# Kernel optimization log

Measured on AMD Instinct MI355X. Metric: run time of the kernel, lower is better.

Reference implementation:

```python
import jax, jax.numpy as jnp
import numpy as np

EPS = 1e-5

def _ln(t, g, b):
    m = t.mean(-1, keepdims=True)
    v = ((t - m) ** 2).mean(-1, keepdims=True)
    return (t - m) * jax.lax.rsqrt(v + EPS) * g + b

def _sr(t, w, b, H, W, sr):
    # t: [B, H*W, C] -> spatial-reduction conv -> [B, (H//sr)*(W//sr), C]
    B, L, C = t.shape
    xi = t.transpose(0, 2, 1).reshape(B, C, H, W)
    y = jax.lax.conv_general_dilated(xi, w, (sr, sr), 'VALID',
                                     dimension_numbers=('NCHW', 'OIHW', 'NCHW'))
    return y.reshape(B, C, -1).transpose(0, 2, 1) + b

def setup_inputs() -> dict:
    key = jax.random.key(0)
    ks = jax.random.split(key, 9)
    C, head, sr, H, W = 128, 2, 2, 64, 64
    B, N = 4, 2 * H * W
    s = 0.02
    return {
        'x': jax.random.normal(ks[0], (B, N, C), jnp.float32),
        'qW': jax.random.normal(ks[1], (C, C), jnp.float32) * s,
        'qb': jnp.zeros((C,), jnp.float32),
        'kvW': jax.random.normal(ks[2], (C, 2 * C), jnp.float32) * s,
        'kvb': jnp.zeros((2 * C,), jnp.float32),
        'projW': jax.random.normal(ks[3], (C, C), jnp.float32) * s,
        'projb': jnp.zeros((C,), jnp.float32),
        'srW': jax.random.normal(ks[4], (C, C, sr, sr), jnp.float32) * s,
        'srb': jnp.zeros((C,), jnp.float32),
        'lnW': jnp.ones((C,), jnp.float32),
        'lnB': jnp.zeros((C,), jnp.float32),
        'H': H, 'W': W, 'fuse': 1,
    }

def reference(x, qW, qb, kvW, kvb, projW, projb, srW, srb, lnW, lnB, H, W, fuse):
    head, sr = 2, 2
    B, N, C = x.shape
    Dh = C // head
    scale = Dh ** -0.5
    q = (x @ qW + qb).reshape(B, N, head, Dh).transpose(0, 2, 1, 3)  # [B,h,N,Dh]
    mask = None
    if fuse and sr > 1:
        half = N // 2
        x_rgb = _ln(_sr(x[:, :half, :], srW, srb, H, W, sr), lnW, lnB)
        x_dte = _ln(_sr(x[:, half:, :], srW, srb, H, W, sr), lnW, lnB)
        xkv = jnp.concatenate([x_rgb, x_dte], axis=1)
        M = N // (sr * sr)
        row = jnp.arange(N)[:, None] < half            # query in rgb half
        col = jnp.arange(M)[None, :] < (M // 2)        # key in rgb half
        mask = row == col                              # True on same-modality blocks -> masked
    elif sr > 1:
        xkv = _ln(_sr(x, srW, srb, H, W, sr), lnW, lnB)
    else:
        xkv = x
    M = xkv.shape[1]
    kv = (xkv @ kvW + kvb).reshape(B, M, 2, head, Dh).transpose(2, 0, 3, 1, 4)
    k, v = kv[0], kv[1]                                # [B,h,M,Dh]
    attn = jnp.einsum('bhnd,bhmd->bhnm', q, k) * scale
    if mask is not None:
        attn = jnp.where(mask[None, None], -jnp.inf, attn)
    attn = jax.nn.softmax(attn, axis=-1)
    out = jnp.einsum('bhnm,bhmd->bhnd', attn, v).transpose(0, 2, 1, 3).reshape(B, N, C)
    return out @ projW + projb
```

## Files before the change

kernel.cpp:

```cpp
#include <hip/hip_runtime.h>
#include <hip/hip_bf16.h>

#define LN_EPS 1e-5f

typedef __attribute__((ext_vector_type(8))) short bf16x8_t;
typedef __attribute__((ext_vector_type(4))) short bf16x4_t;
typedef __attribute__((ext_vector_type(4))) float f32x4_t;
typedef __attribute__((ext_vector_type(4))) unsigned short u16x4_t;

#define MFMA32(a, b, c) __builtin_amdgcn_mfma_f32_16x16x32_bf16(a, b, c, 0, 0, 0)
#define MFMA16(a, b, c) __builtin_amdgcn_mfma_f32_16x16x16bf16_1k(a, b, c, 0, 0, 0)

__device__ inline unsigned short f2bf(float f) {
    union { float f; unsigned int u; } v; v.f = f;
    unsigned int r = v.u + 0x7fffu + ((v.u >> 16) & 1u);
    return (unsigned short)(r >> 16);
}

__device__ inline u16x4_t pk4(float a, float b, float c, float d) {
    union { u16x4_t v; __hip_bfloat162 h[2]; } u;
    u.h[0] = __float22bfloat162_rn(float2{a, b});
    u.h[1] = __float22bfloat162_rn(float2{c, d});
    return u.v;
}
__device__ inline bf16x4_t pk4b(float a, float b, float c, float d) {
    union { bf16x4_t v; __hip_bfloat162 h[2]; } u;
    u.h[0] = __float22bfloat162_rn(float2{a, b});
    u.h[1] = __float22bfloat162_rn(float2{c, d});
    return u.v;
}
__device__ inline bf16x8_t pk8(float4 a, float4 b) {
    union { bf16x8_t v; __hip_bfloat162 h[4]; } u;
    u.h[0] = __float22bfloat162_rn(float2{a.x, a.y});
    u.h[1] = __float22bfloat162_rn(float2{a.z, a.w});
    u.h[2] = __float22bfloat162_rn(float2{b.x, b.y});
    u.h[3] = __float22bfloat162_rn(float2{b.z, b.w});
    return u.v;
}

__device__ inline size_t fragidx(int row, int k, int KC) {
    return ((size_t)((row >> 4) * KC + (k >> 5))) * 512 +
           (((k >> 3) & 3) * 16 + (row & 15)) * 8 + (k & 7);
}

__global__ void k_prep_w(const float* __restrict__ qW, const float* __restrict__ kvW,
                         const float* __restrict__ projW, const float* __restrict__ srW,
                         unsigned short* __restrict__ qWs, unsigned short* __restrict__ kvWs,
                         unsigned short* __restrict__ projWs, unsigned short* __restrict__ srWs) {
    int i = blockIdx.x * 256 + threadIdx.x;
    if (i < 16384) {
        int n = i & 127, k = i >> 7;
        qWs[fragidx(n, k, 4)] = f2bf(qW[k * 128 + n]);
    } else if (i < 49152) {
        int j = i - 16384; int n = j & 255, k = j >> 8;
        kvWs[fragidx(n, k, 4)] = f2bf(kvW[k * 256 + n]);
    } else if (i < 65536) {
        int j = i - 49152; int n = j & 127, k = j >> 7;
        projWs[fragidx(n, k, 4)] = f2bf(projW[k * 128 + n]);
    } else {
        int j = i - 65536; int n = j >> 9, rem = j & 511, q = rem >> 7, c = rem & 127;
        srWs[fragidx(n, q * 128 + c, 16)] = f2bf(srW[n * 512 + c * 4 + q]);
    }
}

__global__ __launch_bounds__(256)
void k_convkv(const float* __restrict__ x, const unsigned short* __restrict__ srWs,
              const float* __restrict__ srb, const float* __restrict__ lnW,
              const float* __restrict__ lnB, const unsigned short* __restrict__ kvWs,
              const float* __restrict__ kvb, unsigned short* __restrict__ ksw,
              unsigned short* __restrict__ vls) {
    const int t = threadIdx.x, w = t >> 6, lane = t & 63;
    const int col = lane & 15, quad = lane >> 4;
    const int RT = blockIdx.x;

    __shared__ unsigned short xs[4 * 512];
    __shared__ float lnred[4][16][2];

    const int pos = RT * 16 + col;
    const int pb = pos >> 11, phf = (pos >> 10) & 1;
    const int poy = (pos >> 5) & 31, pox = pos & 31;
    int rowbase[4];
    #pragma unroll
    for (int q = 0; q < 4; q++) {
        int ky = q >> 1, kx = q & 1;
        int n = phf * 4096 + (2 * poy + ky) * 64 + 2 * pox + kx;
        rowbase[q] = (pb * 8192 + n) * 128;
    }

    f32x4_t acc[2] = {};
    {
        const unsigned short* wp = srWs + lane * 8;
        #pragma unroll
        for (int kc = 0; kc < 16; kc++) {
            const float* xr = x + rowbase[kc >> 2] + (kc & 3) * 32 + quad * 8;
            float4 xa = *(const float4*)(xr);
            float4 xb2 = *(const float4*)(xr + 4);
            bf16x8_t xb = pk8(xa, xb2);
            #pragma unroll
            for (int jj = 0; jj < 2; jj++) {
                bf16x8_t wf = *(const bf16x8_t*)(wp + (size_t)((w * 2 + jj) * 16 + kc) * 512);
                acc[jj] = MFMA32(wf, xb, acc[jj]);
            }
        }
    }
    float s = 0.f, ss = 0.f;
    #pragma unroll
    for (int jj = 0; jj < 2; jj++) {
        float4 bs = *(const float4*)(srb + (w * 2 + jj) * 16 + quad * 4);
        acc[jj][0] += bs.x; acc[jj][1] += bs.y; acc[jj][2] += bs.z; acc[jj][3] += bs.w;
        #pragma unroll
        for (int r = 0; r < 4; r++) { float v = acc[jj][r]; s += v; ss += v * v; }
    }
    s += __shfl_xor(s, 16, 64);  s += __shfl_xor(s, 32, 64);
    ss += __shfl_xor(ss, 16, 64); ss += __shfl_xor(ss, 32, 64);
    if (lane < 16) { lnred[w][lane][0] = s; lnred[w][lane][1] = ss; }
    __syncthreads();
    float stot = 0.f, sstot = 0.f;
    #pragma unroll
    for (int ww = 0; ww < 4; ww++) { stot += lnred[ww][col][0]; sstot += lnred[ww][col][1]; }
    float mean = stot * (1.0f / 128.0f);
    float var = sstot * (1.0f / 128.0f) - mean * mean;
    float rs = rsqrtf(var + LN_EPS);
    #pragma unroll
    for (int jj = 0; jj < 2; jj++) {
        int f0 = (w * 2 + jj) * 16 + quad * 4;
        float4 g = *(const float4*)(lnW + f0);
        float4 be = *(const float4*)(lnB + f0);
        u16x4_t o = pk4((acc[jj][0] - mean) * rs * g.x + be.x,
                        (acc[jj][1] - mean) * rs * g.y + be.y,
                        (acc[jj][2] - mean) * rs * g.z + be.z,
                        (acc[jj][3] - mean) * rs * g.w + be.w);
        *(u16x4_t*)(xs + ((size_t)(f0 >> 5)) * 512 +
                    (((f0 >> 3) & 3) * 16 + col) * 8 + (f0 & 7)) = o;
    }
    __syncthreads();
    bf16x8_t xf[4];
    #pragma unroll
    for (int kc = 0; kc < 4; kc++)
        xf[kc] = *(const bf16x8_t*)(xs + (size_t)kc * 512 + lane * 8);
    const int p0 = RT * 16;
    const int bb = p0 >> 11;
    #pragma unroll
    for (int jj = 0; jj < 2; jj++) {
        const int nt = w * 2 + jj;
        f32x4_t aK = {};
        #pragma unroll
        for (int kc = 0; kc < 4; kc++) {
            bf16x8_t wf = *(const bf16x8_t*)(kvWs + (size_t)(nt * 4 + kc) * 512 + lane * 8);
            aK = MFMA32(wf, xf[kc], aK);
        }
        float4 bs = *(const float4*)(kvb + nt * 16 + quad * 4);
        int m = (p0 + col) & 2047;
        int bh = bb * 2 + (nt >> 2);
        int d0 = (nt & 3) * 16 + quad * 4;
        u16x4_t o = pk4(aK[0] + bs.x, aK[1] + bs.y, aK[2] + bs.z, aK[3] + bs.w);
        *(u16x4_t*)(ksw + ((size_t)(bh * 128 + (m >> 4)) * 2 + (d0 >> 5)) * 512 +
                    (((d0 >> 3) & 3) * 16 + (m & 15)) * 8 + (d0 & 7)) = o;
    }
    #pragma unroll
    for (int jj = 0; jj < 2; jj++) {
        const int nt = w * 2 + jj;
        f32x4_t aV = {};
        #pragma unroll
        for (int kc = 0; kc < 4; kc++) {
            bf16x8_t wf = *(const bf16x8_t*)(kvWs + (size_t)((8 + nt) * 4 + kc) * 512 + lane * 8);
            aV = MFMA32(xf[kc], wf, aV);
        }
        int fv = nt * 16 + col;
        int h = fv >> 6, dd = fv & 63;
        float bv = kvb[128 + fv];
        int m0 = (p0 + quad * 4) & 2047;
        int bh = bb * 2 + h;
        int kt = m0 >> 6, nb = (m0 >> 4) & 3;
        u16x4_t o = pk4(aV[0] + bv, aV[1] + bv, aV[2] + bv, aV[3] + bv);
        *(u16x4_t*)(vls + (((size_t)(bh * 32 + kt) * 4 + (dd >> 4)) * 2 + (nb >> 1)) * 512 +
                    (quad * 16 + (dd & 15)) * 8 + (nb & 1) * 4) = o;
    }
}

__global__ __launch_bounds__(256)
void k_attn_f3(const float* __restrict__ x, const unsigned short* __restrict__ qWs,
               const float* __restrict__ qb, const unsigned short* __restrict__ ksw,
               const unsigned short* __restrict__ vls, const unsigned short* __restrict__ projWs,
               const float* __restrict__ projb, float* __restrict__ out) {
    const int blkx = blockIdx.x, mod = blockIdx.y, b = blockIdx.z;
    const int t = threadIdx.x, w = t >> 6, lane = t & 63;
    const int col = lane & 15, quad = lane >> 4;
    const int h = w & 1, ks = w >> 1;
    const int bh = b * 2 + h;
    const int qbase = mod * 4096 + blkx * 32;

    __shared__ float Ocomb[2 * 32 * 64];
    __shared__ float lcomb[64];
    __shared__ unsigned short rows[32 * 136];
    __shared__ unsigned short qfr[2 * 4 * 512];

    {
        const int qt = ks;
        const float* xrow = x + ((size_t)b * 8192 + qbase + qt * 16 + col) * 128;
        const float sc = 0.125f * 1.44269504089f;
        f32x4_t acc[4] = {};
        #pragma unroll
        for (int kc = 0; kc < 4; kc++) {
            float4 xa = *(const float4*)(xrow + kc * 32 + quad * 8);
            float4 xb2 = *(const float4*)(xrow + kc * 32 + quad * 8 + 4);
            bf16x8_t xf = pk8(xa, xb2);
            #pragma unroll
            for (int j = 0; j < 4; j++) {
                bf16x8_t wf = *(const bf16x8_t*)(qWs + (size_t)((h * 4 + j) * 4 + kc) * 512 + lane * 8);
                acc[j] = MFMA32(wf, xf, acc[j]);
            }
        }
        #pragma unroll
        for (int j = 0; j < 4; j++) {
            float4 bs = *(const float4*)(qb + h * 64 + j * 16 + quad * 4);
            u16x4_t o = pk4((acc[j][0] + bs.x) * sc, (acc[j][1] + bs.y) * sc,
                            (acc[j][2] + bs.z) * sc, (acc[j][3] + bs.w) * sc);
            *(u16x4_t*)(qfr + (size_t)h * 2048 + ((size_t)(qt * 2 + (j >> 1))) * 512 +
                        (((j & 1) * 2 + (quad >> 1)) * 16 + col) * 8 + (quad & 1) * 4) = o;
        }
    }
    __syncthreads();
    bf16x8_t qf[2][2];
    #pragma unroll
    for (int qt = 0; qt < 2; qt++)
        #pragma unroll
        for (int kc = 0; kc < 2; kc++)
            qf[qt][kc] = *(const bf16x8_t*)(qfr + (size_t)h * 2048 +
                                            (size_t)(qt * 2 + kc) * 512 + lane * 8);

    const unsigned short* kp0 =
        ksw + ((size_t)(bh * 128 + (1 - mod) * 64) * 2) * 512 + lane * 8;
    const unsigned short* vp0 =
        vls + ((size_t)(bh * 32 + (1 - mod) * 16) * 8) * 512 + lane * 8;
    const bf16x4_t ones4 = { 0x3F80, 0x3F80, 0x3F80, 0x3F80 };

    f32x4_t O[2][4] = {};
    f32x4_t accl[2] = {};

    for (int kt = ks * 8; kt < ks * 8 + 8; kt++) {
        bf16x8_t kf[8];
        #pragma unroll
        for (int i = 0; i < 8; i++)
            kf[i] = *(const bf16x8_t*)(kp0 + (size_t)(kt * 8 + i) * 512);
        union { bf16x8_t v8; bf16x4_t v4[2]; } vf[8];
        #pragma unroll
        for (int i = 0; i < 8; i++)
            vf[i].v8 = *(const bf16x8_t*)(vp0 + (size_t)(kt * 8 + i) * 512);
        f32x4_t ST[2][4];
        #pragma unroll
        for (int qt = 0; qt < 2; qt++)
            #pragma unroll
            for (int nb = 0; nb < 4; nb++) {
                f32x4_t sA = {};
                sA = MFMA32(kf[nb * 2 + 0], qf[qt][0], sA);
                sA = MFMA32(kf[nb * 2 + 1], qf[qt][1], sA);
                ST[qt][nb] = sA;
            }
        bf16x4_t pa[2][4];
        #pragma unroll
        for (int qt = 0; qt < 2; qt++)
            #pragma unroll
            for (int nb = 0; nb < 4; nb++)
                pa[qt][nb] = pk4b(exp2f(ST[qt][nb][0]), exp2f(ST[qt][nb][1]),
                                  exp2f(ST[qt][nb][2]), exp2f(ST[qt][nb][3]));
        #pragma unroll
        for (int qt = 0; qt < 2; qt++) {
            #pragma unroll
            for (int nb = 0; nb < 4; nb++) {
                accl[qt] = MFMA16(pa[qt][nb], ones4, accl[qt]);
                #pragma unroll
                for (int dt = 0; dt < 4; dt++)
                    O[qt][dt] = MFMA16(pa[qt][nb], vf[dt * 2 + (nb >> 1)].v4[nb & 1], O[qt][dt]);
            }
        }
    }

    if (ks == 1) {
        #pragma unroll
        for (int qt = 0; qt < 2; qt++)
            #pragma unroll
            for (int r = 0; r < 4; r++) {
                int qrow = qt * 16 + quad * 4 + r;
                #pragma unroll
                for (int dt = 0; dt < 4; dt++)
                    Ocomb[(h * 32 + qrow) * 64 + dt * 16 + col] = O[qt][dt][r];
                if (col == 0) lcomb[h * 32 + qrow] = accl[qt][r];
            }
    }
    __syncthreads();
    if (ks == 0) {
        #pragma unroll
        for (int qt = 0; qt < 2; qt++)
            #pragma unroll
            for (int r = 0; r < 4; r++) {
                int qrow = qt * 16 + quad * 4 + r;
                float lt = accl[qt][r] + lcomb[h * 32 + qrow];
                float rl = 1.0f / lt;
                #pragma unroll
                for (int dt = 0; dt < 4; dt++) {
                    float ov = O[qt][dt][r] + Ocomb[(h * 32 + qrow) * 64 + dt * 16 + col];
                    rows[qrow * 136 + h * 64 + dt * 16 + col] = f2bf(ov * rl);
                }
            }
    }
    __syncthreads();
    if (ks == 0) {
        const int qt2 = h;
        bf16x8_t ob[4];
        #pragma unroll
        for (int kc = 0; kc < 4; kc++)
            ob[kc] = *(const bf16x8_t*)(rows + (size_t)(qt2 * 16 + col) * 136 + kc * 32 + quad * 8);
        f32x4_t acc[8];
        #pragma unroll
        for (int j = 0; j < 8; j++) acc[j] = f32x4_t{};
        #pragma unroll
        for (int kc = 0; kc < 4; kc++)
            #pragma unroll
            for (int j = 0; j < 8; j++) {
                bf16x8_t wf = *(const bf16x8_t*)(projWs + (size_t)(j * 4 + kc) * 512 + lane * 8);
                acc[j] = MFMA32(wf, ob[kc], acc[j]);
            }
        const int n = b * 8192 + qbase + qt2 * 16 + col;
        #pragma unroll
        for (int j = 0; j < 8; j++) {
            int f0 = j * 16 + quad * 4;
            float4 bs = *(const float4*)(projb + f0);
            float4 o = { acc[j][0] + bs.x, acc[j][1] + bs.y,
                         acc[j][2] + bs.z, acc[j][3] + bs.w };
            *(float4*)(out + (size_t)n * 128 + f0) = o;
        }
    }
}

extern "C" void kernel_launch(void* const* d_in, const int* in_sizes, int n_in,
                              void* d_out, int out_size, void* d_ws, size_t ws_size,
                              hipStream_t stream) {
    const float* x     = (const float*)d_in[0];
    const float* qW    = (const float*)d_in[1];
    const float* qb    = (const float*)d_in[2];
    const float* kvW   = (const float*)d_in[3];
    const float* kvb   = (const float*)d_in[4];
    const float* projW = (const float*)d_in[5];
    const float* projb = (const float*)d_in[6];
    const float* srW   = (const float*)d_in[7];
    const float* srb   = (const float*)d_in[8];
    const float* lnW   = (const float*)d_in[9];
    const float* lnB   = (const float*)d_in[10];

    char* ws = (char*)d_ws;
    unsigned short* qWs    = (unsigned short*)(ws + 0);
    unsigned short* kvWs   = (unsigned short*)(ws + 32768);
    unsigned short* projWs = (unsigned short*)(ws + 98304);
    unsigned short* srWs   = (unsigned short*)(ws + 131072);
    unsigned short* ksw    = (unsigned short*)(ws + 262144);
    unsigned short* vls    = (unsigned short*)(ws + 2359296);

    k_prep_w<<<dim3(512), dim3(256), 0, stream>>>(qW, kvW, projW, srW,
                                                  qWs, kvWs, projWs, srWs);
    k_convkv<<<dim3(512), dim3(256), 0, stream>>>(x, srWs, srb, lnW, lnB,
                                                  kvWs, kvb, ksw, vls);
    k_attn_f3<<<dim3(128, 2, 4), dim3(256), 0, stream>>>(x, qWs, qb, ksw, vls,
                                                         projWs, projb, (float*)d_out);
}
```

Baseline: 149.5 us.

## Stage K/V tiles in double-buffered LDS shared across query groups

The attention kernel now handles 64 queries per block instead of 32. Each of the four waves owns one (query group, head) pair and processes the full key range, so the split-K partial-sum combine is gone. K and V tiles are loaded cooperatively into a 64KB double-buffered LDS arena, with a register prefetch of the next tile, so the two query groups reuse each tile instead of each fetching it from global memory. The cost is a __syncthreads per key tile, a large LDS footprint that limits occupancy, and half as many blocks in the grid.

After: 147.8 us. Within noise of the previous version (-1.1%).

```diff
diff --git a/kernel.cpp b/kernel.cpp
--- a/kernel.cpp
+++ b/kernel.cpp
@@ -179,26 +179,24 @@
 }
 
 __global__ __launch_bounds__(256)
-void k_attn_f3(const float* __restrict__ x, const unsigned short* __restrict__ qWs,
+void k_attn_f4(const float* __restrict__ x, const unsigned short* __restrict__ qWs,
                const float* __restrict__ qb, const unsigned short* __restrict__ ksw,
                const unsigned short* __restrict__ vls, const unsigned short* __restrict__ projWs,
                const float* __restrict__ projb, float* __restrict__ out) {
     const int blkx = blockIdx.x, mod = blockIdx.y, b = blockIdx.z;
     const int t = threadIdx.x, w = t >> 6, lane = t & 63;
     const int col = lane & 15, quad = lane >> 4;
-    const int h = w & 1, ks = w >> 1;
-    const int bh = b * 2 + h;
-    const int qbase = mod * 4096 + blkx * 32;
-
-    __shared__ float Ocomb[2 * 32 * 64];
-    __shared__ float lcomb[64];
-    __shared__ unsigned short rows[32 * 136];
-    __shared__ unsigned short qfr[2 * 4 * 512];
-
-    {
-        const int qt = ks;
+    const int qg = w & 1, h = w >> 1;
+    const int qbase = mod * 4096 + blkx * 64 + qg * 32;
+
+    __shared__ char arena[65536];
+    unsigned short* sbuf = (unsigned short*)arena;
+
+    unsigned short* qarea = sbuf + w * 2048;
+    const float sc = 0.125f * 1.44269504089f;
+    #pragma unroll
+    for (int qt = 0; qt < 2; qt++) {
         const float* xrow = x + ((size_t)b * 8192 + qbase + qt * 16 + col) * 128;
-        const float sc = 0.125f * 1.44269504089f;
         f32x4_t acc[4] = {};
         #pragma unroll
         for (int kc = 0; kc < 4; kc++) {
@@ -216,37 +214,59 @@
             float4 bs = *(const float4*)(qb + h * 64 + j * 16 + quad * 4);
             u16x4_t o = pk4((acc[j][0] + bs.x) * sc, (acc[j][1] + bs.y) * sc,
                             (acc[j][2] + bs.z) * sc, (acc[j][3] + bs.w) * sc);
-            *(u16x4_t*)(qfr + (size_t)h * 2048 + ((size_t)(qt * 2 + (j >> 1))) * 512 +
+            *(u16x4_t*)(qarea + ((size_t)(qt * 2 + (j >> 1))) * 512 +
                         (((j & 1) * 2 + (quad >> 1)) * 16 + col) * 8 + (quad & 1) * 4) = o;
         }
     }
-    __syncthreads();
     bf16x8_t qf[2][2];
     #pragma unroll
     for (int qt = 0; qt < 2; qt++)
         #pragma unroll
         for (int kc = 0; kc < 2; kc++)
-            qf[qt][kc] = *(const bf16x8_t*)(qfr + (size_t)h * 2048 +
-                                            (size_t)(qt * 2 + kc) * 512 + lane * 8);
-
-    const unsigned short* kp0 =
-        ksw + ((size_t)(bh * 128 + (1 - mod) * 64) * 2) * 512 + lane * 8;
-    const unsigned short* vp0 =
-        vls + ((size_t)(bh * 32 + (1 - mod) * 16) * 8) * 512 + lane * 8;
+            qf[qt][kc] = *(const bf16x8_t*)(qarea + (size_t)(qt * 2 + kc) * 512 + lane * 8);
+    __syncthreads();
+
+    const int rh = w & 1;
+    const int bhr = b * 2 + rh;
+    const unsigned short* src0 = (w < 2)
+        ? ksw + ((size_t)(bhr * 128 + (1 - mod) * 64) * 2) * 512
+        : vls + ((size_t)(bhr * 32 + (1 - mod) * 16) * 8) * 512;
+    const int regoff = (w < 2 ? 0 : 16384) + rh * 8192;
+
+    const int bh = b * 2 + h;
+    (void)bh;
     const bf16x4_t ones4 = { 0x3F80, 0x3F80, 0x3F80, 0x3F80 };
 
     f32x4_t O[2][4] = {};
     f32x4_t accl[2] = {};
 
-    for (int kt = ks * 8; kt < ks * 8 + 8; kt++) {
+    bf16x8_t pre[8];
+    #pragma unroll
+    for (int cc = 0; cc < 8; cc++)
+        pre[cc] = *(const bf16x8_t*)(src0 + (size_t)cc * 512 + lane * 8);
+    #pragma unroll
+    for (int cc = 0; cc < 8; cc++)
+        *(bf16x8_t*)(arena + regoff + cc * 1024 + lane * 16) = pre[cc];
+    __syncthreads();
+
+    int buf = 0;
+    for (int kt = 0; kt < 16; kt++) {
+        if (kt < 15) {
+            const unsigned short* s = src0 + (size_t)(kt + 1) * 4096 + lane * 8;
+            #pragma unroll
+            for (int cc = 0; cc < 8; cc++)
+                pre[cc] = *(const bf16x8_t*)(s + (size_t)cc * 512);
+        }
+        const char* kbase = arena + buf * 32768 + h * 8192;
+        const char* vbase = arena + buf * 32768 + 16384 + h * 8192;
         bf16x8_t kf[8];
         #pragma unroll
         for (int i = 0; i < 8; i++)
-            kf[i] = *(const bf16x8_t*)(kp0 + (size_t)(kt * 8 + i) * 512);
+            kf[i] = *(const bf16x8_t*)(kbase + i * 1024 + lane * 16);
         union { bf16x8_t v8; bf16x4_t v4[2]; } vf[8];
         #pragma unroll
         for (int i = 0; i < 8; i++)
-            vf[i].v8 = *(const bf16x8_t*)(vp0 + (size_t)(kt * 8 + i) * 512);
+            vf[i].v8 = *(const bf16x8_t*)(vbase + i * 1024 + lane * 16);
         f32x4_t ST[2][4];
         #pragma unroll
         for (int qt = 0; qt < 2; qt++)
@@ -274,43 +294,34 @@
                     O[qt][dt] = MFMA16(pa[qt][nb], vf[dt * 2 + (nb >> 1)].v4[nb & 1], O[qt][dt]);
             }
         }
-    }
-
-    if (ks == 1) {
-        #pragma unroll
-        for (int qt = 0; qt < 2; qt++)
-            #pragma unroll
-            for (int r = 0; r < 4; r++) {
-                int qrow = qt * 16 + quad * 4 + r;
-                #pragma unroll
-                for (int dt = 0; dt < 4; dt++)
-                    Ocomb[(h * 32 + qrow) * 64 + dt * 16 + col] = O[qt][dt][r];
-                if (col == 0) lcomb[h * 32 + qrow] = accl[qt][r];
-            }
-    }
-    __syncthreads();
-    if (ks == 0) {
-        #pragma unroll
-        for (int qt = 0; qt < 2; qt++)
-            #pragma unroll
-            for (int r = 0; r < 4; r++) {
-                int qrow = qt * 16 + quad * 4 + r;
-                float lt = accl[qt][r] + lcomb[h * 32 + qrow];
-                float rl = 1.0f / lt;
-                #pragma unroll
-                for (int dt = 0; dt < 4; dt++) {
-                    float ov = O[qt][dt][r] + Ocomb[(h * 32 + qrow) * 64 + dt * 16 + col];
-                    rows[qrow * 136 + h * 64 + dt * 16 + col] = f2bf(ov * rl);
-                }
-            }
-    }
-    __syncthreads();
-    if (ks == 0) {
-        const int qt2 = h;
+        if (kt < 15) {
+            char* d = arena + (buf ^ 1) * 32768 + regoff;
+            #pragma unroll
+            for (int cc = 0; cc < 8; cc++)
+                *(bf16x8_t*)(d + cc * 1024 + lane * 16) = pre[cc];
+        }
+        __syncthreads();
+        buf ^= 1;
+    }
+
+    #pragma unroll
+    for (int qt = 0; qt < 2; qt++) {
+        #pragma unroll
+        for (int r = 0; r < 4; r++) {
+            float rl = 1.0f / accl[qt][r];
+            int qrow = qg * 32 + qt * 16 + quad * 4 + r;
+            #pragma unroll
+            for (int dt = 0; dt < 4; dt++)
+                sbuf[qrow * 136 + h * 64 + dt * 16 + col] = f2bf(O[qt][dt][r] * rl);
+        }
+    }
+    __syncthreads();
+    {
+        const int qt2 = w;
         bf16x8_t ob[4];
         #pragma unroll
         for (int kc = 0; kc < 4; kc++)
-            ob[kc] = *(const bf16x8_t*)(rows + (size_t)(qt2 * 16 + col) * 136 + kc * 32 + quad * 8);
+            ob[kc] = *(const bf16x8_t*)(sbuf + (size_t)(qt2 * 16 + col) * 136 + kc * 32 + quad * 8);
         f32x4_t acc[8];
         #pragma unroll
         for (int j = 0; j < 8; j++) acc[j] = f32x4_t{};
@@ -321,7 +332,7 @@
                 bf16x8_t wf = *(const bf16x8_t*)(projWs + (size_t)(j * 4 + kc) * 512 + lane * 8);
                 acc[j] = MFMA32(wf, ob[kc], acc[j]);
             }
-        const int n = b * 8192 + qbase + qt2 * 16 + col;
+        const int n = b * 8192 + mod * 4096 + blkx * 64 + qt2 * 16 + col;
         #pragma unroll
         for (int j = 0; j < 8; j++) {
             int f0 = j * 16 + quad * 4;
@@ -360,6 +371,6 @@
                                                   qWs, kvWs, projWs, srWs);
     k_convkv<<<dim3(512), dim3(256), 0, stream>>>(x, srWs, srb, lnW, lnB,
                                                   kvWs, kvb, ksw, vls);
-    k_attn_f3<<<dim3(128, 2, 4), dim3(256), 0, stream>>>(x, qWs, qb, ksw, vls,
-                                                         projWs, projb, (float*)d_out);
-}
+    k_attn_f4<<<dim3(64, 2, 4), dim3(256), 0, stream>>>(x, qWs, qb, ksw, vls,
+                                                        projWs, projb, (float*)d_out);
+}
```
